# Performance work log

Measured on AMD Instinct MI355X. Metric: run time of the kernel, lower is better.

Reference implementation:

```python
import jax, jax.numpy as jnp
import numpy as np

D = 256
H = 16
HD = D // H
N_BIAS = 6
B, E = 8, 1024


def _layernorm(x, g, b, eps=1e-5):
    mu = jnp.mean(x, axis=-1, keepdims=True)
    var = jnp.mean(jnp.square(x - mu), axis=-1, keepdims=True)
    return (x - mu) * jax.lax.rsqrt(var + eps) * g + b


def setup_inputs() -> dict:
    key = jax.random.key(0)
    ks = jax.random.split(key, 16)
    s = 0.02
    inp = {
        "x": jax.random.normal(ks[0], (B, E, D), dtype=jnp.float32),
        "struct_bias": jax.random.randint(ks[1], (B, E, E), 0, N_BIAS),
        "key_padding_mask": jnp.zeros((B, E), dtype=bool),
        # projections stored as [in, out] so y = x @ W + b
        "Wq": jax.random.normal(ks[2], (D, D), jnp.float32) * s,
        "bq": jnp.zeros((D,), jnp.float32),
        "Wk": jax.random.normal(ks[3], (D, D), jnp.float32) * s,
        "bk": jnp.zeros((D,), jnp.float32),
        "Wv": jax.random.normal(ks[4], (D, D), jnp.float32) * s,
        "bv": jnp.zeros((D,), jnp.float32),
        "Wo": jax.random.normal(ks[5], (D, D), jnp.float32) * s,
        "bo": jnp.zeros((D,), jnp.float32),
        "bias_emb": jax.random.normal(ks[6], (N_BIAS, H), jnp.float32) * s,
        "ln1_g": jnp.ones((D,), jnp.float32),
        "ln1_b": jnp.zeros((D,), jnp.float32),
        "W_ff1": jax.random.normal(ks[7], (D, 4 * D), jnp.float32) * s,
        "b_ff1": jnp.zeros((4 * D,), jnp.float32),
        "W_ff2": jax.random.normal(ks[8], (4 * D, D), jnp.float32) * s,
        "b_ff2": jnp.zeros((D,), jnp.float32),
        "ln2_g": jnp.ones((D,), jnp.float32),
        "ln2_b": jnp.zeros((D,), jnp.float32),
    }
    return inp


def reference(x, struct_bias, key_padding_mask, Wq, bq, Wk, bk, Wv, bv, Wo, bo,
              bias_emb, ln1_g, ln1_b, W_ff1, b_ff1, W_ff2, b_ff2, ln2_g, ln2_b):
    b, e, d = x.shape
    # project and split heads: [B, H, E, HD]
    q = (x @ Wq + bq).reshape(b, e, H, HD).transpose(0, 2, 1, 3)
    k = (x @ Wk + bk).reshape(b, e, H, HD).transpose(0, 2, 1, 3)
    v = (x @ Wv + bv).reshape(b, e, H, HD).transpose(0, 2, 1, 3)
    scores = jnp.einsum('bhqd,bhkd->bhqk', q, k) / np.sqrt(HD).astype(np.float32)
    # learned structural bias: [B,E,E,H] -> [B,H,E,E]
    bias = bias_emb[struct_bias].transpose(0, 3, 1, 2)
    scores = scores + bias
    scores = jnp.where(key_padding_mask[:, None, None, :], -jnp.inf, scores)
    attn = jax.nn.softmax(scores, axis=-1)
    out = jnp.einsum('bhqk,bhkd->bhqd', attn, v)
    out = out.transpose(0, 2, 1, 3).reshape(b, e, d)
    out = out @ Wo + bo
    x = _layernorm(x + out, ln1_g, ln1_b)
    ff = jax.nn.gelu(x @ W_ff1 + b_ff1, approximate=False) @ W_ff2 + b_ff2
    x = _layernorm(x + ff, ln2_g, ln2_b)
    return x
```

## Files before the change

### kernel.cpp

```cpp
#include <hip/hip_runtime.h>
#include <math.h>

#define B_  8
#define E_  1024
#define D_  256
#define H_  16
#define FF_ 1024
#define M_  (B_ * E_)

typedef __attribute__((ext_vector_type(8))) short short8;
typedef __attribute__((ext_vector_type(4))) float f32x4;
typedef unsigned short bf16u;

#define GLOAD_LDS16(g, l) __builtin_amdgcn_global_load_lds( \
    (const __attribute__((address_space(1))) void*)(g), \
    (__attribute__((address_space(3))) void*)(l), 16, 0, 0)

__device__ __forceinline__ unsigned short f2bf(float f) {
  union { float f; unsigned u; } c; c.f = f;
  unsigned r = c.u + 0x7fffu + ((c.u >> 16) & 1u);
  return (unsigned short)(r >> 16);
}
__device__ __forceinline__ float gelu_exact(float x) {
  return 0.5f * x * (1.0f + erff(x * 0.70710678118654752f));
}

template<int BM, int BN, int EPI>
__global__ __launch_bounds__(256) void mm_k(
    const bf16u* __restrict__ A, const bf16u* __restrict__ Wt,
    const float* __restrict__ bias, const float* __restrict__ R,
    void* __restrict__ Cout, int M, int N, int K)
{
  constexpr int WM = BM / 2, WN = BN / 2;
  constexpr int MT = WM / 16, NT = WN / 16;
  constexpr int PA = BM * 8 / 256, PB = BN * 8 / 256;
  constexpr int LBM = (BM == 128 ? 7 : 6), LBN = (BN == 128 ? 7 : 6);
  __shared__ bf16u As[BM * 64];
  __shared__ bf16u Bs[BN * 64];

  const int t = threadIdx.x;
  const int l15 = t & 15, quad = (t >> 4) & 3;
  const int w = t >> 6, wm = w >> 1, wn = w & 1;
  const int m0 = blockIdx.x * BM, n0 = blockIdx.y * BN;

  f32x4 acc[MT][NT];
  const f32x4 z4 = {0.f, 0.f, 0.f, 0.f};
#pragma unroll
  for (int i = 0; i < MT; ++i)
#pragma unroll
    for (int j = 0; j < NT; ++j) acc[i][j] = z4;

  for (int k0 = 0; k0 < K; k0 += 64) {
    __syncthreads();
#pragma unroll
    for (int p = 0; p < PA; ++p) {
      int g = p * 256 + t;
      int m = g & (BM - 1), c = g >> LBM;
      const bf16u* src = A + (size_t)(m0 + m) * K + k0 + c * 8;
      GLOAD_LDS16(src, As + g * 8);
    }
#pragma unroll
    for (int p = 0; p < PB; ++p) {
      int g = p * 256 + t;
      int n = g & (BN - 1), c = g >> LBN;
      const bf16u* src = Wt + (size_t)(n0 + n) * K + k0 + c * 8;
      GLOAD_LDS16(src, Bs + g * 8);
    }
    __syncthreads();
#pragma unroll
    for (int s = 0; s < 2; ++s) {
      short8 af[MT], bfr[NT];
#pragma unroll
      for (int mt = 0; mt < MT; ++mt)
        af[mt] = *(const short8*)(As + ((s * 4 + quad) * BM + wm * WM + mt * 16 + l15) * 8);
#pragma unroll
      for (int nt = 0; nt < NT; ++nt)
        bfr[nt] = *(const short8*)(Bs + ((s * 4 + quad) * BN + wn * WN + nt * 16 + l15) * 8);
#pragma unroll
      for (int mt = 0; mt < MT; ++mt)
#pragma unroll
        for (int nt = 0; nt < NT; ++nt)
          acc[mt][nt] = __builtin_amdgcn_mfma_f32_16x16x32_bf16(
              af[mt], bfr[nt], acc[mt][nt], 0, 0, 0);
    }
  }

#pragma unroll
  for (int mt = 0; mt < MT; ++mt) {
#pragma unroll
    for (int nt = 0; nt < NT; ++nt) {
      int col = n0 + wn * WN + nt * 16 + l15;
      float bia = bias[col];
#pragma unroll
      for (int r = 0; r < 4; ++r) {
        int row = m0 + wm * WM + mt * 16 + quad * 4 + r;
        size_t idx = (size_t)row * N + col;
        float v = acc[mt][nt][r] + bia;
        if (EPI == 1)      { ((float*)Cout)[idx] = v + R[idx]; }
        else if (EPI == 2) { ((bf16u*)Cout)[idx] = f2bf(gelu_exact(v)); }
        else               { ((bf16u*)Cout)[idx] = f2bf(v); }
      }
    }
  }
}

__global__ __launch_bounds__(256) void prep_k(
    const float* __restrict__ Wq, const float* __restrict__ Wk,
    const float* __restrict__ Wv, const float* __restrict__ Wo,
    const float* __restrict__ Wf1, const float* __restrict__ Wf2,
    bf16u* __restrict__ Wqkvt, bf16u* __restrict__ Wot,
    bf16u* __restrict__ Wf1t, bf16u* __restrict__ Wf2t,
    const float* __restrict__ bq, const float* __restrict__ bk,
    const float* __restrict__ bv, float* __restrict__ bqkv,
    const float* __restrict__ X, bf16u* __restrict__ Xb)
{
  __shared__ float tile[32][33];
  const int gid = blockIdx.x;
  const int t = threadIdx.x;

  if (gid < 768) {
    const float* src; bf16u* dst; int K, N, bx, by;
    if (gid < 256) {
      const int z = gid >> 6, r = gid & 63;
      src = (z == 0) ? Wq : (z == 1) ? Wk : (z == 2) ? Wv : Wo;
      dst = (z == 0) ? Wqkvt : (z == 1) ? Wqkvt + 65536
          : (z == 2) ? Wqkvt + 131072 : Wot;
      K = 256; N = 256; bx = r & 7; by = r >> 3;
    } else if (gid < 512) {
      const int r = gid - 256;
      src = Wf1; dst = Wf1t; K = 256; N = 1024; bx = r & 7; by = r >> 3;
    } else {
      const int r = gid - 512;
      src = Wf2; dst = Wf2t; K = 1024; N = 256; bx = r & 31; by = r >> 5;
    }
    const int tx = t & 31, ty = t >> 5;
    const int kb = bx * 32, nb = by * 32;
#pragma unroll
    for (int r = 0; r < 4; ++r)
      tile[ty + 8 * r][tx] = src[(size_t)(kb + ty + 8 * r) * N + nb + tx];
    __syncthreads();
#pragma unroll
    for (int r = 0; r < 4; ++r)
      dst[(size_t)(nb + ty + 8 * r) * K + kb + tx] = f2bf(tile[tx][ty + 8 * r]);
  } else if (gid < 771) {
    int i = (gid - 768) * 256 + t;
    bqkv[i] = (i < 256) ? bq[i] : (i < 512) ? bk[i - 256] : bv[i - 512];
  } else {
    int i = (gid - 771) * 256 + t;
    float4 a = ((const float4*)X)[i * 2];
    float4 b = ((const float4*)X)[i * 2 + 1];
    uint4 o;
    o.x = f2bf(a.x) | ((unsigned)f2bf(a.y) << 16);
    o.y = f2bf(a.z) | ((unsigned)f2bf(a.w) << 16);
    o.z = f2bf(b.x) | ((unsigned)f2bf(b.y) << 16);
    o.w = f2bf(b.z) | ((unsigned)f2bf(b.w) << 16);
    ((uint4*)Xb)[i] = o;
  }
}

__global__ __launch_bounds__(256) void attn_k(
    const bf16u* __restrict__ qkv, const int* __restrict__ sb,
    const unsigned char* __restrict__ mask, const float* __restrict__ be,
    bf16u* __restrict__ O)
{
  __shared__ bf16u Kl[2][64][40];
  __shared__ bf16u Vt[2][2][16][40];
  __shared__ float emb2[6][2];

  const int t    = threadIdx.x;
  const int b    = blockIdx.z;
  const int hg   = blockIdx.y;
  const int w    = t >> 6;
  const int lane = t & 63;
  const int l15  = lane & 15;
  const int quad = lane >> 4;
  const int q0w  = blockIdx.x * 64 + w * 16;
  const float C2 = 0.36067376022224085f;

  if (t < 12) emb2[t >> 1][t & 1] = be[(t >> 1) * 16 + hg * 2 + (t & 1)] * 1.44269504088896f;

  {
    float4 z = {0.f, 0.f, 0.f, 0.f};
    float4* kp = (float4*)&Kl[0][0][0];
    for (int i = t; i < 640; i += 256) kp[i] = z;
  }

  short8 qf[2];
#pragma unroll
  for (int hp = 0; hp < 2; ++hp) {
    uint4 v = {0u, 0u, 0u, 0u};
    if (quad < 2)
      v = *(const uint4*)(qkv + ((size_t)(b * E_) + q0w + l15) * 768 +
                          (hg * 2 + hp) * 16 + quad * 8);
    else if (quad == 2)
      v.x = 0x3F80u;
    union { uint4 u; short8 s; } c; c.u = v;
    qf[hp] = c.s;
  }

  const int s_hp   = t >> 7;
  const int s_key  = (t >> 1) & 63;
  const int s_half = t & 1;
  const int v_hp   = t >> 7;
  const int vu     = t & 127;
  const int vz     = vu >> 2;
  const int vh     = (vu >> 1) & 1;
  const int vjh    = vu & 1;
  const int vs2    = vz >> 4;
  const int vrow0  = vh * 8 + vjh * 4;
  const int vc     = ((vz >> 1) & 3) * 8 + ((vz >> 3) & 1) * 4 + (vz & 1) * 2;

  const size_t kvbase = (size_t)b * E_ * 768;
  const bf16u* kbase = qkv + kvbase + 256 + (hg * 2 + s_hp) * 16 + s_half * 8;
  const bf16u* vbase = qkv + kvbase + 512 + (hg * 2 + v_hp) * 16 + vrow0;
  const int* sbp = sb + ((size_t)(b * E_) + q0w) * E_;

  f32x4 accO[2];
  const f32x4 z4 = {0.f, 0.f, 0.f, 0.f};
  accO[0] = z4; accO[1] = z4;
  float lsum[2] = {0.f, 0.f};

  for (int k0 = 0; k0 < E_; k0 += 64) {
    int sraw[2][2][4];
#pragma unroll
    for (int s2 = 0; s2 < 2; ++s2)
#pragma unroll
      for (int kb = 0; kb < 2; ++kb)
        *(int4*)&sraw[s2][kb][0] =
            *(const int4*)(sbp + (size_t)l15 * E_ + k0 + s2 * 32 + kb * 16 + quad * 4);

    __syncthreads();
    {
      *(uint4*)&Kl[s_hp][s_key][s_half * 8] =
          *(const uint4*)(kbase + (size_t)(k0 + s_key) * 768);
      if (s_half == 0)
        Kl[s_hp][s_key][16] = mask[b * E_ + k0 + s_key] ? (bf16u)0xCF6E : (bf16u)0;
      const bf16u* p0 = vbase + (size_t)(k0 + 2 * vz) * 768;
      union { uint2 u; bf16u e[4]; } va, vb;
      va.u = *(const uint2*)p0;
      vb.u = *(const uint2*)(p0 + 768);
#pragma unroll
      for (int j = 0; j < 4; ++j)
        *(unsigned*)&Vt[v_hp][vs2][vrow0 + j][vc] =
            (unsigned)va.e[j] | ((unsigned)vb.e[j] << 16);
    }
    __syncthreads();

#pragma unroll
    for (int s2 = 0; s2 < 2; ++s2) {
      short8 k00 = *(const short8*)&Kl[0][s2 * 32 + l15][quad * 8];
      short8 k01 = *(const short8*)&Kl[0][s2 * 32 + 16 + l15][quad * 8];
      short8 k10 = *(const short8*)&Kl[1][s2 * 32 + l15][quad * 8];
      short8 k11 = *(const short8*)&Kl[1][s2 * 32 + 16 + l15][quad * 8];
      f32x4 sc00 = __builtin_amdgcn_mfma_f32_16x16x32_bf16(k00, qf[0], z4, 0, 0, 0);
      f32x4 sc01 = __builtin_amdgcn_mfma_f32_16x16x32_bf16(k01, qf[0], z4, 0, 0, 0);
      f32x4 sc10 = __builtin_amdgcn_mfma_f32_16x16x32_bf16(k10, qf[1], z4, 0, 0, 0);
      f32x4 sc11 = __builtin_amdgcn_mfma_f32_16x16x32_bf16(k11, qf[1], z4, 0, 0, 0);

      unsigned pk0[4], pk1[4];
#pragma unroll
      for (int r = 0; r < 4; ++r) {
        float2 w0 = *(const float2*)&emb2[sraw[s2][0][r]][0];
        float2 w1 = *(const float2*)&emb2[sraw[s2][1][r]][0];
        float p00 = __builtin_amdgcn_exp2f(fmaf(sc00[r], C2, w0.x));
        float p01 = __builtin_amdgcn_exp2f(fmaf(sc01[r], C2, w1.x));
        float p10 = __builtin_amdgcn_exp2f(fmaf(sc10[r], C2, w0.y));
        float p11 = __builtin_amdgcn_exp2f(fmaf(sc11[r], C2, w1.y));
        unsigned u00 = __float_as_uint(p00), u01 = __float_as_uint(p01);
        unsigned u10 = __float_as_uint(p10), u11 = __float_as_uint(p11);
        lsum[0] += __uint_as_float(u00 & 0xffff0000u) + __uint_as_float(u01 & 0xffff0000u);
        lsum[1] += __uint_as_float(u10 & 0xffff0000u) + __uint_as_float(u11 & 0xffff0000u);
        if ((r & 1) == 0) {
          pk0[r >> 1]       = u00 >> 16;
          pk0[2 + (r >> 1)] = u01 >> 16;
          pk1[r >> 1]       = u10 >> 16;
          pk1[2 + (r >> 1)] = u11 >> 16;
        } else {
          pk0[r >> 1]       |= u00 & 0xffff0000u;
          pk0[2 + (r >> 1)] |= u01 & 0xffff0000u;
          pk1[r >> 1]       |= u10 & 0xffff0000u;
          pk1[2 + (r >> 1)] |= u11 & 0xffff0000u;
        }
      }
      union { unsigned u[4]; short8 s; } a0, a1;
      a0.u[0] = pk0[0]; a0.u[1] = pk0[1]; a0.u[2] = pk0[2]; a0.u[3] = pk0[3];
      a1.u[0] = pk1[0]; a1.u[1] = pk1[1]; a1.u[2] = pk1[2]; a1.u[3] = pk1[3];

      short8 vf0 = *(const short8*)&Vt[0][s2][l15][quad * 8];
      short8 vf1 = *(const short8*)&Vt[1][s2][l15][quad * 8];
      accO[0] = __builtin_amdgcn_mfma_f32_16x16x32_bf16(a0.s, vf0, accO[0], 0, 0, 0);
      accO[1] = __builtin_amdgcn_mfma_f32_16x16x32_bf16(a1.s, vf1, accO[1], 0, 0, 0);
    }
  }

#pragma unroll
  for (int hp = 0; hp < 2; ++hp) {
    lsum[hp] += __shfl_xor(lsum[hp], 16, 64);
    lsum[hp] += __shfl_xor(lsum[hp], 32, 64);
  }
#pragma unroll
  for (int hp = 0; hp < 2; ++hp) {
#pragma unroll
    for (int r = 0; r < 4; ++r) {
      float lq = __shfl(lsum[hp], quad * 4 + r, 64);
      float o = accO[hp][r] / lq;
      O[((size_t)(b * E_) + q0w + quad * 4 + r) * 256 + (hg * 2 + hp) * 16 + l15] = f2bf(o);
    }
  }
}

template<int DUAL>
__global__ __launch_bounds__(256) void ln_k(
    const float* __restrict__ X, const float* __restrict__ g,
    const float* __restrict__ bta, float* __restrict__ Y, bf16u* __restrict__ Yb)
{
  const int row  = blockIdx.x * 4 + (threadIdx.x >> 6);
  const int lane = threadIdx.x & 63;
  float4 v = *(const float4*)(X + (size_t)row * D_ + lane * 4);
  float s  = v.x + v.y + v.z + v.w;
  float ss = v.x * v.x + v.y * v.y + v.z * v.z + v.w * v.w;
#pragma unroll
  for (int off = 32; off; off >>= 1) {
    s  += __shfl_xor(s, off, 64);
    ss += __shfl_xor(ss, off, 64);
  }
  float mu  = s * (1.f / 256.f);
  float var = ss * (1.f / 256.f) - mu * mu;
  float rs  = 1.f / sqrtf(var + 1e-5f);
  float4 gv = *(const float4*)(g + lane * 4);
  float4 bv = *(const float4*)(bta + lane * 4);
  float4 o;
  o.x = (v.x - mu) * rs * gv.x + bv.x;
  o.y = (v.y - mu) * rs * gv.y + bv.y;
  o.z = (v.z - mu) * rs * gv.z + bv.z;
  o.w = (v.w - mu) * rs * gv.w + bv.w;
  *(float4*)(Y + (size_t)row * D_ + lane * 4) = o;
  if (DUAL) {
    uint2 p;
    p.x = f2bf(o.x) | ((unsigned)f2bf(o.y) << 16);
    p.y = f2bf(o.z) | ((unsigned)f2bf(o.w) << 16);
    *(uint2*)(Yb + (size_t)row * D_ + lane * 4) = p;
  }
}

extern "C" void kernel_launch(void* const* d_in, const int* in_sizes, int n_in,
                              void* d_out, int out_size, void* d_ws, size_t ws_size,
                              hipStream_t stream) {
  const float* x   = (const float*)d_in[0];
  const int*   sb  = (const int*)d_in[1];
  const unsigned char* mask = (const unsigned char*)d_in[2];
  const float* Wq  = (const float*)d_in[3];
  const float* bq  = (const float*)d_in[4];
  const float* Wk  = (const float*)d_in[5];
  const float* bk  = (const float*)d_in[6];
  const float* Wv  = (const float*)d_in[7];
  const float* bv  = (const float*)d_in[8];
  const float* Wo  = (const float*)d_in[9];
  const float* bo  = (const float*)d_in[10];
  const float* be  = (const float*)d_in[11];
  const float* g1  = (const float*)d_in[12];
  const float* b1  = (const float*)d_in[13];
  const float* Wf1 = (const float*)d_in[14];
  const float* bf1 = (const float*)d_in[15];
  const float* Wf2 = (const float*)d_in[16];
  const float* bf2 = (const float*)d_in[17];
  const float* g2  = (const float*)d_in[18];
  const float* b2  = (const float*)d_in[19];
  float* out = (float*)d_out;

  char* ws = (char*)d_ws;
  bf16u* Wqkvt = (bf16u*)(ws + 0);
  bf16u* Wot   = (bf16u*)(ws + 393216);
  bf16u* Wf1t  = (bf16u*)(ws + 524288);
  bf16u* Wf2t  = (bf16u*)(ws + 1048576);
  float* bqkv  = (float*)(ws + 1572864);
  bf16u* xb    = (bf16u*)(ws + 2097152);
  bf16u* qkv   = (bf16u*)(ws + 6291456);
  bf16u* att   = (bf16u*)(ws + 18874368);
  float* t1    = (float*)(ws + 23068672);
  float* x1    = (float*)(ws + 31457280);
  bf16u* x1b   = (bf16u*)(ws + 39845888);
  bf16u* ffh   = (bf16u*)(ws + 2097152);
  float* t2    = (float*)(ws + 18874368);

  dim3 blk(256);

  prep_k<<<1795, blk, 0, stream>>>(Wq, Wk, Wv, Wo, Wf1, Wf2,
                                   Wqkvt, Wot, Wf1t, Wf2t,
                                   bq, bk, bv, bqkv, x, xb);

  mm_k<128, 128, 0><<<dim3(64, 6), blk, 0, stream>>>(xb, Wqkvt, bqkv, nullptr,
                                                     qkv, M_, 768, 256);
  attn_k<<<dim3(16, 8, 8), blk, 0, stream>>>(qkv, sb, mask, be, att);

  mm_k<64, 64, 1><<<dim3(128, 4), blk, 0, stream>>>(att, Wot, bo, x,
                                                    t1, M_, 256, 256);
  ln_k<1><<<M_ / 4, blk, 0, stream>>>(t1, g1, b1, x1, x1b);

  mm_k<128, 128, 2><<<dim3(64, 8), blk, 0, stream>>>(x1b, Wf1t, bf1, nullptr,
                                                     ffh, M_, 1024, 256);
  mm_k<64, 64, 1><<<dim3(128, 4), blk, 0, stream>>>(ffh, Wf2t, bf2, x1,
                                                    t2, M_, 256, 1024);
  ln_k<0><<<M_ / 4, blk, 0, stream>>>(t2, g2, b2, out, nullptr);
}
```

Measured before the change: 234.3 us.

## Double-buffer K/V shared tiles and prefetch next tile into registers

The attention kernel's K/V LDS tiles become double-buffered. The next iteration's K, V, mask and struct-bias values are loaded into registers before the current tile's MFMA and softmax work, then written to the alternate buffer at the top of the next iteration. This removes one of the two barriers per tile and overlaps global-load latency with compute. In exchange it doubles LDS usage and raises register pressure from the prefetched operands, which may lower occupancy.

```diff
diff --git a/kernel.cpp b/kernel.cpp
--- a/kernel.cpp
+++ b/kernel.cpp
@@ -163,8 +163,8 @@
     const unsigned char* __restrict__ mask, const float* __restrict__ be,
     bf16u* __restrict__ O)
 {
-  __shared__ bf16u Kl[2][64][40];
-  __shared__ bf16u Vt[2][2][16][40];
+  __shared__ bf16u Kl[2][2][64][40];
+  __shared__ bf16u Vt[2][2][2][16][40];
   __shared__ float emb2[6][2];
 
   const int t    = threadIdx.x;
@@ -181,8 +181,8 @@
 
   {
     float4 z = {0.f, 0.f, 0.f, 0.f};
-    float4* kp = (float4*)&Kl[0][0][0];
-    for (int i = t; i < 640; i += 256) kp[i] = z;
+    float4* kp = (float4*)&Kl[0][0][0][0];
+    for (int i = t; i < 1280; i += 256) kp[i] = z;
   }
 
   short8 qf[2];
@@ -201,7 +201,6 @@
   const int s_hp   = t >> 7;
   const int s_key  = (t >> 1) & 63;
   const int s_half = t & 1;
-  const int v_hp   = t >> 7;
   const int vu     = t & 127;
   const int vz     = vu >> 2;
   const int vh     = (vu >> 1) & 1;
@@ -212,46 +211,72 @@
 
   const size_t kvbase = (size_t)b * E_ * 768;
   const bf16u* kbase = qkv + kvbase + 256 + (hg * 2 + s_hp) * 16 + s_half * 8;
-  const bf16u* vbase = qkv + kvbase + 512 + (hg * 2 + v_hp) * 16 + vrow0;
-  const int* sbp = sb + ((size_t)(b * E_) + q0w) * E_;
+  const bf16u* vbase = qkv + kvbase + 512 + (hg * 2 + s_hp) * 16 + vrow0;
+  const int* sbp = sb + ((size_t)(b * E_) + q0w + l15) * E_;
 
   f32x4 accO[2];
   const f32x4 z4 = {0.f, 0.f, 0.f, 0.f};
   accO[0] = z4; accO[1] = z4;
   float lsum[2] = {0.f, 0.f};
 
-  for (int k0 = 0; k0 < E_; k0 += 64) {
-    int sraw[2][2][4];
+  uint4 kA;
+  uint2 va, vb;
+  unsigned mA;
+  int sraw[2][2][4];
+  {
+    kA = *(const uint4*)(kbase + (size_t)s_key * 768);
+    const bf16u* p0 = vbase + (size_t)(2 * vz) * 768;
+    va = *(const uint2*)p0;
+    vb = *(const uint2*)(p0 + 768);
+    mA = mask[b * E_ + s_key];
 #pragma unroll
     for (int s2 = 0; s2 < 2; ++s2)
 #pragma unroll
-      for (int kb = 0; kb < 2; ++kb)
-        *(int4*)&sraw[s2][kb][0] =
-            *(const int4*)(sbp + (size_t)l15 * E_ + k0 + s2 * 32 + kb * 16 + quad * 4);
+      for (int kb2 = 0; kb2 < 2; ++kb2)
+        *(int4*)&sraw[s2][kb2][0] =
+            *(const int4*)(sbp + s2 * 32 + kb2 * 16 + quad * 4);
+  }
+  __syncthreads();
+
+#pragma unroll 2
+  for (int i = 0; i < 16; ++i) {
+    const int cur = i & 1;
+
+    *(uint4*)&Kl[cur][s_hp][s_key][s_half * 8] = kA;
+    {
+      union { uint2 u; bf16u e[4]; } a, c; a.u = va; c.u = vb;
+#pragma unroll
+      for (int j = 0; j < 4; ++j)
+        *(unsigned*)&Vt[cur][s_hp][vs2][vrow0 + j][vc] =
+            (unsigned)a.e[j] | ((unsigned)c.e[j] << 16);
+    }
+    if (s_half == 0)
+      Kl[cur][s_hp][s_key][16] = mA ? (bf16u)0xCF6E : (bf16u)0;
 
     __syncthreads();
-    {
-      *(uint4*)&Kl[s_hp][s_key][s_half * 8] =
-          *(const uint4*)(kbase + (size_t)(k0 + s_key) * 768);
-      if (s_half == 0)
-        Kl[s_hp][s_key][16] = mask[b * E_ + k0 + s_key] ? (bf16u)0xCF6E : (bf16u)0;
-      const bf16u* p0 = vbase + (size_t)(k0 + 2 * vz) * 768;
-      union { uint2 u; bf16u e[4]; } va, vb;
-      va.u = *(const uint2*)p0;
-      vb.u = *(const uint2*)(p0 + 768);
-#pragma unroll
-      for (int j = 0; j < 4; ++j)
-        *(unsigned*)&Vt[v_hp][vs2][vrow0 + j][vc] =
-            (unsigned)va.e[j] | ((unsigned)vb.e[j] << 16);
-    }
-    __syncthreads();
+
+    int srn[2][2][4];
+    if (i < 15) {
+      const int kn = (i + 1) * 64;
+      kA = *(const uint4*)(kbase + (size_t)(kn + s_key) * 768);
+      const bf16u* p0 = vbase + (size_t)(kn + 2 * vz) * 768;
+      va = *(const uint2*)p0;
+      vb = *(const uint2*)(p0 + 768);
+      mA = mask[b * E_ + kn + s_key];
+#pragma unroll
+      for (int s2 = 0; s2 < 2; ++s2)
+#pragma unroll
+        for (int kb2 = 0; kb2 < 2; ++kb2)
+          *(int4*)&srn[s2][kb2][0] =
+              *(const int4*)(sbp + kn + s2 * 32 + kb2 * 16 + quad * 4);
+    }
 
 #pragma unroll
     for (int s2 = 0; s2 < 2; ++s2) {
-      short8 k00 = *(const short8*)&Kl[0][s2 * 32 + l15][quad * 8];
-      short8 k01 = *(const short8*)&Kl[0][s2 * 32 + 16 + l15][quad * 8];
-      short8 k10 = *(const short8*)&Kl[1][s2 * 32 + l15][quad * 8];
-      short8 k11 = *(const short8*)&Kl[1][s2 * 32 + 16 + l15][quad * 8];
+      short8 k00 = *(const short8*)&Kl[cur][0][s2 * 32 + l15][quad * 8];
+      short8 k01 = *(const short8*)&Kl[cur][0][s2 * 32 + 16 + l15][quad * 8];
+      short8 k10 = *(const short8*)&Kl[cur][1][s2 * 32 + l15][quad * 8];
+      short8 k11 = *(const short8*)&Kl[cur][1][s2 * 32 + 16 + l15][quad * 8];
       f32x4 sc00 = __builtin_amdgcn_mfma_f32_16x16x32_bf16(k00, qf[0], z4, 0, 0, 0);
       f32x4 sc01 = __builtin_amdgcn_mfma_f32_16x16x32_bf16(k01, qf[0], z4, 0, 0, 0);
       f32x4 sc10 = __builtin_amdgcn_mfma_f32_16x16x32_bf16(k10, qf[1], z4, 0, 0, 0);
@@ -286,10 +311,20 @@
       a0.u[0] = pk0[0]; a0.u[1] = pk0[1]; a0.u[2] = pk0[2]; a0.u[3] = pk0[3];
       a1.u[0] = pk1[0]; a1.u[1] = pk1[1]; a1.u[2] = pk1[2]; a1.u[3] = pk1[3];
 
-      short8 vf0 = *(const short8*)&Vt[0][s2][l15][quad * 8];
-      short8 vf1 = *(const short8*)&Vt[1][s2][l15][quad * 8];
+      short8 vf0 = *(const short8*)&Vt[cur][0][s2][l15][quad * 8];
+      short8 vf1 = *(const short8*)&Vt[cur][1][s2][l15][quad * 8];
       accO[0] = __builtin_amdgcn_mfma_f32_16x16x32_bf16(a0.s, vf0, accO[0], 0, 0, 0);
       accO[1] = __builtin_amdgcn_mfma_f32_16x16x32_bf16(a1.s, vf1, accO[1], 0, 0, 0);
+    }
+
+    if (i < 15) {
+#pragma unroll
+      for (int s2 = 0; s2 < 2; ++s2)
+#pragma unroll
+        for (int kb2 = 0; kb2 < 2; ++kb2)
+#pragma unroll
+          for (int r = 0; r < 4; ++r)
+            sraw[s2][kb2][r] = srn[s2][kb2][r];
     }
   }
 
```

Result: no change. 229.7 us (-2.0%).
